# Performance work log

Measured on AMD Instinct MI355X. Metric: run time of the kernel, lower is better.

Reference implementation:

```python
import jax, jax.numpy as jnp
import numpy as np

ITERS = 15
KERNEL = 7
PAD = 3
INIT_RATE = 0.1
SCALE_PSDF = 1000.0
EDGE_THRESH = 0.01


def _min_pool7(x):
    # torch: -maxpool2d(-x, k=7, s=1, p=3)  ==  min-pool, padding with +inf
    return jax.lax.reduce_window(
        x, jnp.inf, jax.lax.min,
        window_dimensions=(1, 1, KERNEL, KERNEL),
        window_strides=(1, 1, 1, 1),
        padding=[(0, 0), (0, 0), (PAD, PAD), (PAD, PAD)])


def _erode_weight(mask):
    # FaceWeightedFusion.obtain_face_mask_weight: 15-iter erosion, each shell
    # of pixels removed at iteration i gets weight init_rate + i*(1-init_rate)/15
    mask_erode = mask
    mask_final = jnp.zeros_like(mask)
    for i in range(ITERS):
        nxt = _min_pool7(mask_erode)
        rate = min(INIT_RATE + i * ((1.0 - INIT_RATE) / ITERS), 1.0)
        mask_final = mask_final + (mask_erode - nxt) * rate
        mask_erode = nxt
    return mask_final + mask_erode


def _bilinear_sample(img, xy):
    # img: [B,1,H,W]; xy: [B,2,N] in [-1,1] (grid_sample convention, align_corners=True)
    B, _, H, W = img.shape
    x = (xy[:, 0] + 1.0) * 0.5 * (W - 1)  # [B,N]
    y = (xy[:, 1] + 1.0) * 0.5 * (H - 1)
    x0 = jnp.floor(x); y0 = jnp.floor(y)
    wx = x - x0; wy = y - y0
    x0i = jnp.clip(x0, 0, W - 1).astype(jnp.int32)
    x1i = jnp.clip(x0 + 1, 0, W - 1).astype(jnp.int32)
    y0i = jnp.clip(y0, 0, H - 1).astype(jnp.int32)
    y1i = jnp.clip(y0 + 1, 0, H - 1).astype(jnp.int32)
    flat = img[:, 0].reshape(B, H * W)
    g = lambda yi, xi: jnp.take_along_axis(flat, yi * W + xi, axis=1)
    v = (g(y0i, x0i) * (1 - wx) * (1 - wy) + g(y0i, x1i) * wx * (1 - wy)
         + g(y1i, x0i) * (1 - wx) * wy + g(y1i, x1i) * wx * wy)
    return v[:, None, :]  # [B,1,N]


def setup_inputs() -> dict:
    key = jax.random.key(0)
    ks = jax.random.split(key, 7)
    B, H, W, N = 4, 1024, 1024, 262144
    mask = (jax.random.uniform(ks[0], (B, 1, H, W)) > 0.5).astype(jnp.float32)
    face_depth = jax.random.uniform(ks[1], (B, 1, H, W))
    face_depth_edge_mask = (jax.random.uniform(ks[2], (B, 1, H, W)) > 0.3).astype(jnp.float32)
    xy = jax.random.uniform(ks[3], (B, 2, N)) * 2.0 - 1.0
    z = jax.random.normal(ks[4], (B, 1, N)) * 0.1 + 0.5
    occ_body = jax.random.uniform(ks[5], (B, 1, N))
    occ_face = jax.random.uniform(ks[6], (B, 1, N))
    return {"mask": mask, "face_depth": face_depth,
            "face_depth_edge_mask": face_depth_edge_mask,
            "xy": xy, "z": z, "occ_body": occ_body, "occ_face": occ_face}


def reference(mask, face_depth, face_depth_edge_mask, xy, z, occ_body, occ_face):
    # obtain_face_mask_weight
    mask_erode = _erode_weight(mask)
    # calculate_fusion_weights (x_weighted=True)
    edge = _bilinear_sample(face_depth_edge_mask, xy)
    edge_b = (edge > EDGE_THRESH).astype(face_depth.dtype)
    depth_q = _bilinear_sample(face_depth, xy) * edge_b
    psdf = z - depth_q
    labels = _bilinear_sample(mask_erode, xy) * edge_b
    w = jnp.exp(-(psdf ** 2) * SCALE_PSDF) * labels
    # fusion(occ_body, occ_face)
    return w * occ_face + (1.0 - w) * occ_body
```

## Files before the change

### kernel.cpp

```cpp
#include <hip/hip_runtime.h>
#include <stdint.h>


#define HH 1024
#define WW 1024
#define HWIMG (HH * WW)
#define NPTS 262144

typedef short short2v __attribute__((ext_vector_type(2)));
typedef float f32x4 __attribute__((ext_vector_type(4)));
typedef uint32_t u32x2 __attribute__((ext_vector_type(2), aligned(4)));

static __device__ __forceinline__ uint32_t umin_(uint32_t a, uint32_t b) { return a < b ? a : b; }

__global__ __launch_bounds__(256) void row_dt_kernel(const float* __restrict__ mask,
                                                     uint8_t* __restrict__ rbuf) {
    const int l = threadIdx.x & 63;
    const int row = blockIdx.x * 4 + (threadIdx.x >> 6);
    const float* mrow = mask + (size_t)row * WW;

    uint64_t bm[18];
    bm[0] = 0ull;
    bm[17] = 0ull;
#pragma unroll
    for (int i = 0; i < 16; ++i) {
        float m = mrow[i * 64 + l];
        bm[i + 1] = __ballot(m == 0.0f);
    }

    uint8_t* rrow = rbuf + (size_t)row * WW;
#pragma unroll
    for (int i = 0; i < 16; ++i) {
        uint64_t W0 = bm[i];
        uint64_t W1 = bm[i + 1];
        uint64_t W2 = bm[i + 2];
        uint64_t rmask = (W1 >> l) | ((W2 << 1) << (63 - l));
        uint64_t lmask = (W1 << (63 - l)) | ((W0 >> 1) >> l);
        int dr = rmask ? __builtin_ctzll(rmask) : 64;
        int dl = lmask ? __builtin_clzll(lmask) : 64;
        int d = dr < dl ? dr : dl;
        if (d > 46) d = 46;
        rrow[i * 64 + l] = (uint8_t)d;
    }
}

template<bool PACK>
__global__ __launch_bounds__(256) void col_dt_kernel(const uint8_t* __restrict__ rbuf,
                                                     const float* __restrict__ edge,
                                                     const float* __restrict__ depth,
                                                     uint8_t* __restrict__ bucket_out,
                                                     uint32_t* __restrict__ packed_out) {
    const int bx = blockIdx.x;
    const int tx = bx & 15, ty = (bx >> 4) & 15, b = bx >> 8;
    const int x0 = tx * 64, y0 = ty * 64;
    const int c = threadIdx.x & 63;
    const int t = threadIdx.x >> 6;
    const int ybase = y0 + t * 16;
    const uint8_t* imgc = rbuf + (size_t)b * HWIMG + x0 + c;

    uint32_t wf[12];
#pragma unroll
    for (int j = 0; j < 12; ++j) {
        int r0 = ybase - 4 + 2 * j;
        int r1 = r0 + 1;
        int r0c = r0 < 0 ? 0 : (r0 > 1023 ? 1023 : r0);
        int r1c = r1 < 0 ? 0 : (r1 > 1023 ? 1023 : r1);
        uint32_t lo = imgc[(size_t)r0c * WW];
        uint32_t hi = imgc[(size_t)r1c * WW];
        if (r0 != r0c) lo = 46;
        if (r1 != r1c) hi = 46;
        wf[j] = lo | (hi << 16);
    }

    uint32_t Dv[16];
    bool bad = false;
#pragma unroll
    for (int i = 0; i < 16; ++i) {
        const int base2 = i >> 1;
        const int par = i & 1;
        short2v D2 = (short2v){46, 46};
#pragma unroll
        for (int q = 0; q < 5; ++q) {
            int dy0 = 2 * q - 4 - par;
            short a0 = (short)(dy0 < 0 ? -dy0 : dy0);
            short a1 = (short)(dy0 + 1 < 0 ? -(dy0 + 1) : dy0 + 1);
            short2v A = (short2v){a0, a1};
            short2v v = __builtin_bit_cast(short2v, wf[base2 + q]);
            short2v mx = __builtin_elementwise_max(A, v);
            D2 = __builtin_elementwise_min(D2, mx);
        }
        uint32_t D = (uint32_t)(D2.x < D2.y ? D2.x : D2.y);
        Dv[i] = D;
        bad |= (D >= 6);
    }

    if (__ballot(bad) != 0) {
#pragma unroll
        for (int i = 0; i < 16; ++i) {
            uint32_t D = 46;
            for (int dy = -46; dy <= 46; ++dy) {
                int y = ybase + i + dy;
                uint32_t r = 46;
                if (y >= 0 && y < HH) r = imgc[(size_t)y * WW];
                uint32_t a = (uint32_t)(dy < 0 ? -dy : dy);
                uint32_t m = a > r ? a : r;
                D = D < m ? D : m;
            }
            Dv[i] = D;
        }
    }

#pragma unroll
    for (int i = 0; i < 16; ++i) {
        uint32_t D = Dv[i];
        const size_t pix = (size_t)b * HWIMG + (size_t)(ybase + i) * WW + x0 + c;
        if (PACK) {
            float dv = __builtin_nontemporal_load(&depth[pix]);
            float ev = __builtin_nontemporal_load(&edge[pix]);
            uint32_t q20 = (uint32_t)fminf(rintf(dv * 1048575.0f), 1048575.0f);
            uint32_t bk = (D == 0) ? 31u : umin_(15u, (D - 1u) / 3u);
            uint32_t word = q20 | (bk << 20) | ((ev != 0.0f ? 1u : 0u) << 25);
            __builtin_nontemporal_store(word, &packed_out[pix]);
        } else {
            uint8_t o = (D == 0) ? (uint8_t)255 : (uint8_t)umin_(15u, (D - 1u) / 3u);
            bucket_out[pix] = o;
        }
    }
}

static __device__ __forceinline__ float decode_w5(uint32_t p) {
    uint32_t k = (p >> 20) & 31u;
    if (k == 31u) return 0.0f;
    float v = 0.1f + (float)k * 0.06f;
    return v < 1.0f ? v : 1.0f;
}

__global__ __launch_bounds__(256) void sample4_kernel(
    const uint32_t* __restrict__ pimg, const float* __restrict__ xy,
    const float* __restrict__ z, const float* __restrict__ occ_body,
    const float* __restrict__ occ_face, float* __restrict__ out) {
    const int b = blockIdx.x & 3;
    const int n0 = (blockIdx.x >> 2) * 1024 + threadIdx.x * 4;
    const size_t pb = (size_t)b * NPTS;

    f32x4 xv  = __builtin_nontemporal_load((const f32x4*)&xy[pb * 2 + n0]);
    f32x4 yv  = __builtin_nontemporal_load((const f32x4*)&xy[pb * 2 + NPTS + n0]);
    f32x4 zv  = __builtin_nontemporal_load((const f32x4*)&z[pb + n0]);
    f32x4 obv = __builtin_nontemporal_load((const f32x4*)&occ_body[pb + n0]);
    f32x4 ofv = __builtin_nontemporal_load((const f32x4*)&occ_face[pb + n0]);

    const uint32_t* img = pimg + (size_t)b * HWIMG;
    f32x4 res;
    const uint32_t* addr[4][2];
    int sel[4];
    float wgt[4][4];
#pragma unroll
    for (int j = 0; j < 4; ++j) {
        float fx = ((xv[j] + 1.0f) * 0.5f) * 1023.0f;
        float fy = ((yv[j] + 1.0f) * 0.5f) * 1023.0f;
        float x0f = floorf(fx), y0f = floorf(fy);
        float wx = fx - x0f, wy = fy - y0f;
        int x0i = (int)x0f; x0i = x0i < 0 ? 0 : (x0i > 1023 ? 1023 : x0i);
        int y0i = (int)y0f; y0i = y0i < 0 ? 0 : (y0i > 1023 ? 1023 : y0i);
        int y1i = y0i + 1 > 1023 ? 1023 : y0i + 1;
        int xl = x0i > 1022 ? 1022 : x0i;
        sel[j] = x0i - xl;
        addr[j][0] = img + (size_t)y0i * WW + xl;
        addr[j][1] = img + (size_t)y1i * WW + xl;
        wgt[j][0] = (1.0f - wx) * (1.0f - wy);
        wgt[j][1] = wx * (1.0f - wy);
        wgt[j][2] = (1.0f - wx) * wy;
        wgt[j][3] = wx * wy;
    }
    u32x2 pr[4][2];
#pragma unroll
    for (int j = 0; j < 4; ++j) {
        pr[j][0] = *(const u32x2*)addr[j][0];
        pr[j][1] = *(const u32x2*)addr[j][1];
    }

#pragma unroll
    for (int j = 0; j < 4; ++j) {
        uint32_t p00 = sel[j] ? pr[j][0].y : pr[j][0].x;
        uint32_t p01 = pr[j][0].y;
        uint32_t p10 = sel[j] ? pr[j][1].y : pr[j][1].x;
        uint32_t p11 = pr[j][1].y;
        float e = (float)((p00 >> 25) & 1u) * wgt[j][0]
                + (float)((p01 >> 25) & 1u) * wgt[j][1]
                + (float)((p10 >> 25) & 1u) * wgt[j][2]
                + (float)((p11 >> 25) & 1u) * wgt[j][3];
        float w = 0.0f;
        if (e > 0.01f) {
            const float DQS = 1.0f / 1048575.0f;
            float dq = ((float)(p00 & 0xFFFFFu) * wgt[j][0]
                      + (float)(p01 & 0xFFFFFu) * wgt[j][1]
                      + (float)(p10 & 0xFFFFFu) * wgt[j][2]
                      + (float)(p11 & 0xFFFFFu) * wgt[j][3]) * DQS;
            float la = decode_w5(p00) * wgt[j][0] + decode_w5(p01) * wgt[j][1]
                     + decode_w5(p10) * wgt[j][2] + decode_w5(p11) * wgt[j][3];
            float ps = zv[j] - dq;
            w = expf(-(ps * ps) * 1000.0f) * la;
        }
        res[j] = w * ofv[j] + (1.0f - w) * obv[j];
    }
    __builtin_nontemporal_store(res, (f32x4*)&out[pb + n0]);
}

static __device__ __forceinline__ float decode_w8(uint32_t k) {
    if (k == 255u) return 0.0f;
    float v = 0.1f + (float)k * 0.06f;
    return v < 1.0f ? v : 1.0f;
}

__global__ __launch_bounds__(256) void sample_fallback_kernel(
    const float* __restrict__ edge_img, const float* __restrict__ depth_img,
    const uint8_t* __restrict__ wimg,
    const float* __restrict__ xy, const float* __restrict__ z,
    const float* __restrict__ occ_body, const float* __restrict__ occ_face,
    float* __restrict__ out) {
    const int b = blockIdx.x & 3;
    const int n = (blockIdx.x >> 2) * 256 + threadIdx.x;

    float x = xy[(size_t)b * 2 * NPTS + n];
    float y = xy[(size_t)b * 2 * NPTS + NPTS + n];
    float fx = ((x + 1.0f) * 0.5f) * 1023.0f;
    float fy = ((y + 1.0f) * 0.5f) * 1023.0f;
    float x0f = floorf(fx), y0f = floorf(fy);
    float wx = fx - x0f, wy = fy - y0f;
    int x0i = (int)x0f; x0i = x0i < 0 ? 0 : (x0i > 1023 ? 1023 : x0i);
    int y0i = (int)y0f; y0i = y0i < 0 ? 0 : (y0i > 1023 ? 1023 : y0i);
    int x1i = x0i + 1 > 1023 ? 1023 : x0i + 1;
    int y1i = y0i + 1 > 1023 ? 1023 : y0i + 1;

    const size_t base = (size_t)b * HWIMG;
    const size_t i00 = base + (size_t)y0i * WW + x0i;
    const size_t i01 = base + (size_t)y0i * WW + x1i;
    const size_t i10 = base + (size_t)y1i * WW + x0i;
    const size_t i11 = base + (size_t)y1i * WW + x1i;

    const float w00 = (1.0f - wx) * (1.0f - wy);
    const float w01 = wx * (1.0f - wy);
    const float w10 = (1.0f - wx) * wy;
    const float w11 = wx * wy;

    float zv = z[(size_t)b * NPTS + n];
    float ob = occ_body[(size_t)b * NPTS + n];
    float of = occ_face[(size_t)b * NPTS + n];

    float w = 0.0f;
    float e = edge_img[i00] * w00 + edge_img[i01] * w01
            + edge_img[i10] * w10 + edge_img[i11] * w11;
    if (e > 0.01f) {
        float dq = depth_img[i00] * w00 + depth_img[i01] * w01
                 + depth_img[i10] * w10 + depth_img[i11] * w11;
        float la = decode_w8(wimg[i00]) * w00 + decode_w8(wimg[i01]) * w01
                 + decode_w8(wimg[i10]) * w10 + decode_w8(wimg[i11]) * w11;
        float ps = zv - dq;
        w = expf(-(ps * ps) * 1000.0f) * la;
    }
    out[(size_t)b * NPTS + n] = w * of + (1.0f - w) * ob;
}

extern "C" void kernel_launch(void* const* d_in, const int* in_sizes, int n_in,
                              void* d_out, int out_size, void* d_ws, size_t ws_size,
                              hipStream_t stream) {
    const float* mask      = (const float*)d_in[0];
    const float* depth     = (const float*)d_in[1];
    const float* edge      = (const float*)d_in[2];
    const float* xy        = (const float*)d_in[3];
    const float* z         = (const float*)d_in[4];
    const float* occ_body  = (const float*)d_in[5];
    const float* occ_face  = (const float*)d_in[6];
    float* out = (float*)d_out;

    uint8_t* rbuf = (uint8_t*)d_ws;
    const size_t need_packed = (size_t)4 * HWIMG + (size_t)4 * HWIMG * 4;

    row_dt_kernel<<<1024, 256, 0, stream>>>(mask, rbuf);

    if (ws_size >= need_packed) {
        uint32_t* pimg = (uint32_t*)(rbuf + (size_t)4 * HWIMG);
        col_dt_kernel<true><<<1024, 256, 0, stream>>>(rbuf, edge, depth, nullptr, pimg);
        sample4_kernel<<<1024, 256, 0, stream>>>(pimg, xy, z, occ_body, occ_face, out);
    } else {
        uint8_t* wbuf = rbuf + (size_t)4 * HWIMG;
        col_dt_kernel<false><<<1024, 256, 0, stream>>>(rbuf, edge, depth, wbuf, nullptr);
        sample_fallback_kernel<<<4096, 256, 0, stream>>>(edge, depth, wbuf,
                                                         xy, z, occ_body, occ_face, out);
    }
}
```

Before: 131.2 us.

## Store packed image as row-pair interleaved planes for single 16-byte bilinear fetch

The column pass now writes the packed depth/edge/weight words into two row-pair interleaved buffers (even-start and odd-start pairs), so each pixel stores its value together with the one below it. The sampler then picks the buffer by row parity and fetches all four bilinear taps with one 16-byte load instead of two 8-byte loads from separate rows. This trades roughly double the packed-image write traffic and workspace for fewer, better-localised random gathers in the sampling kernel.

```diff
diff --git a/kernel.cpp b/kernel.cpp
--- a/kernel.cpp
+++ b/kernel.cpp
@@ -9,7 +9,8 @@
 
 typedef short short2v __attribute__((ext_vector_type(2)));
 typedef float f32x4 __attribute__((ext_vector_type(4)));
-typedef uint32_t u32x2 __attribute__((ext_vector_type(2), aligned(4)));
+typedef uint32_t u32x2 __attribute__((ext_vector_type(2), aligned(8)));
+typedef uint32_t u32x4a __attribute__((ext_vector_type(4), aligned(8)));
 
 static __device__ __forceinline__ uint32_t umin_(uint32_t a, uint32_t b) { return a < b ? a : b; }
 
@@ -49,7 +50,8 @@
                                                      const float* __restrict__ edge,
                                                      const float* __restrict__ depth,
                                                      uint8_t* __restrict__ bucket_out,
-                                                     uint32_t* __restrict__ packed_out) {
+                                                     uint32_t* __restrict__ qE,
+                                                     uint32_t* __restrict__ qO) {
     const int bx = blockIdx.x;
     const int tx = bx & 15, ty = (bx >> 4) & 15, b = bx >> 8;
     const int x0 = tx * 64, y0 = ty * 64;
@@ -110,18 +112,48 @@
         }
     }
 
-#pragma unroll
-    for (int i = 0; i < 16; ++i) {
-        uint32_t D = Dv[i];
-        const size_t pix = (size_t)b * HWIMG + (size_t)(ybase + i) * WW + x0 + c;
-        if (PACK) {
+    if (PACK) {
+        uint32_t wv[16];
+#pragma unroll
+        for (int i = 0; i < 16; ++i) {
+            uint32_t D = Dv[i];
+            const size_t pix = (size_t)b * HWIMG + (size_t)(ybase + i) * WW + x0 + c;
             float dv = __builtin_nontemporal_load(&depth[pix]);
             float ev = __builtin_nontemporal_load(&edge[pix]);
             uint32_t q20 = (uint32_t)fminf(rintf(dv * 1048575.0f), 1048575.0f);
             uint32_t bk = (D == 0) ? 31u : umin_(15u, (D - 1u) / 3u);
-            uint32_t word = q20 | (bk << 20) | ((ev != 0.0f ? 1u : 0u) << 25);
-            __builtin_nontemporal_store(word, &packed_out[pix]);
-        } else {
+            wv[i] = q20 | (bk << 20) | ((ev != 0.0f ? 1u : 0u) << 25);
+        }
+
+        const int xcol = x0 + c;
+        const size_t bq = (size_t)b * (HWIMG / 2);
+        u32x2* qE2 = (u32x2*)qE;
+        u32x2* qO2 = (u32x2*)qO;
+        const int k0 = ybase >> 1;
+#pragma unroll
+        for (int a = 0; a < 8; ++a) {
+            u32x2 pr2 = (u32x2){wv[2 * a], wv[2 * a + 1]};
+            __builtin_nontemporal_store(pr2, &qE2[bq + (size_t)(k0 + a) * WW + xcol]);
+        }
+#pragma unroll
+        for (int a = 0; a < 7; ++a) {
+            u32x2 pr2 = (u32x2){wv[2 * a + 1], wv[2 * a + 2]};
+            __builtin_nontemporal_store(pr2, &qO2[bq + (size_t)(k0 + a) * WW + xcol]);
+        }
+        uint32_t* qOu = qO;
+        const size_t bqu = (size_t)b * HWIMG;
+        if (ybase > 0) {
+            __builtin_nontemporal_store(wv[0], &qOu[bqu + ((size_t)(k0 - 1) * WW + xcol) * 2 + 1]);
+        }
+        __builtin_nontemporal_store(wv[15], &qOu[bqu + ((size_t)(k0 + 7) * WW + xcol) * 2]);
+        if (ybase + 15 == 1023) {
+            __builtin_nontemporal_store(wv[15], &qOu[bqu + ((size_t)(k0 + 7) * WW + xcol) * 2 + 1]);
+        }
+    } else {
+#pragma unroll
+        for (int i = 0; i < 16; ++i) {
+            uint32_t D = Dv[i];
+            const size_t pix = (size_t)b * HWIMG + (size_t)(ybase + i) * WW + x0 + c;
             uint8_t o = (D == 0) ? (uint8_t)255 : (uint8_t)umin_(15u, (D - 1u) / 3u);
             bucket_out[pix] = o;
         }
@@ -136,7 +168,8 @@
 }
 
 __global__ __launch_bounds__(256) void sample4_kernel(
-    const uint32_t* __restrict__ pimg, const float* __restrict__ xy,
+    const uint32_t* __restrict__ qE, const uint32_t* __restrict__ qO,
+    const float* __restrict__ xy,
     const float* __restrict__ z, const float* __restrict__ occ_body,
     const float* __restrict__ occ_face, float* __restrict__ out) {
     const int b = blockIdx.x & 3;
@@ -149,9 +182,9 @@
     f32x4 obv = __builtin_nontemporal_load((const f32x4*)&occ_body[pb + n0]);
     f32x4 ofv = __builtin_nontemporal_load((const f32x4*)&occ_face[pb + n0]);
 
-    const uint32_t* img = pimg + (size_t)b * HWIMG;
+    const size_t bimg = (size_t)b * HWIMG;
     f32x4 res;
-    const uint32_t* addr[4][2];
+    const uint32_t* addr[4];
     int sel[4];
     float wgt[4][4];
 #pragma unroll
@@ -162,29 +195,27 @@
         float wx = fx - x0f, wy = fy - y0f;
         int x0i = (int)x0f; x0i = x0i < 0 ? 0 : (x0i > 1023 ? 1023 : x0i);
         int y0i = (int)y0f; y0i = y0i < 0 ? 0 : (y0i > 1023 ? 1023 : y0i);
-        int y1i = y0i + 1 > 1023 ? 1023 : y0i + 1;
         int xl = x0i > 1022 ? 1022 : x0i;
         sel[j] = x0i - xl;
-        addr[j][0] = img + (size_t)y0i * WW + xl;
-        addr[j][1] = img + (size_t)y1i * WW + xl;
+        const uint32_t* base = (y0i & 1) ? qO : qE;
+        addr[j] = base + bimg + ((size_t)(y0i >> 1) * WW + xl) * 2;
         wgt[j][0] = (1.0f - wx) * (1.0f - wy);
         wgt[j][1] = wx * (1.0f - wy);
         wgt[j][2] = (1.0f - wx) * wy;
         wgt[j][3] = wx * wy;
     }
-    u32x2 pr[4][2];
+    u32x4a pr[4];
 #pragma unroll
     for (int j = 0; j < 4; ++j) {
-        pr[j][0] = *(const u32x2*)addr[j][0];
-        pr[j][1] = *(const u32x2*)addr[j][1];
+        pr[j] = *(const u32x4a*)addr[j];
     }
 
 #pragma unroll
     for (int j = 0; j < 4; ++j) {
-        uint32_t p00 = sel[j] ? pr[j][0].y : pr[j][0].x;
-        uint32_t p01 = pr[j][0].y;
-        uint32_t p10 = sel[j] ? pr[j][1].y : pr[j][1].x;
-        uint32_t p11 = pr[j][1].y;
+        uint32_t p00 = sel[j] ? pr[j].z : pr[j].x;
+        uint32_t p01 = pr[j].z;
+        uint32_t p10 = sel[j] ? pr[j].w : pr[j].y;
+        uint32_t p11 = pr[j].w;
         float e = (float)((p00 >> 25) & 1u) * wgt[j][0]
                 + (float)((p01 >> 25) & 1u) * wgt[j][1]
                 + (float)((p10 >> 25) & 1u) * wgt[j][2]
@@ -274,17 +305,18 @@
     float* out = (float*)d_out;
 
     uint8_t* rbuf = (uint8_t*)d_ws;
-    const size_t need_packed = (size_t)4 * HWIMG + (size_t)4 * HWIMG * 4;
+    const size_t need_packed = (size_t)4 * HWIMG * (1 + 4 + 4);
 
     row_dt_kernel<<<1024, 256, 0, stream>>>(mask, rbuf);
 
     if (ws_size >= need_packed) {
-        uint32_t* pimg = (uint32_t*)(rbuf + (size_t)4 * HWIMG);
-        col_dt_kernel<true><<<1024, 256, 0, stream>>>(rbuf, edge, depth, nullptr, pimg);
-        sample4_kernel<<<1024, 256, 0, stream>>>(pimg, xy, z, occ_body, occ_face, out);
+        uint32_t* qE = (uint32_t*)(rbuf + (size_t)4 * HWIMG);
+        uint32_t* qO = qE + (size_t)4 * HWIMG;
+        col_dt_kernel<true><<<1024, 256, 0, stream>>>(rbuf, edge, depth, nullptr, qE, qO);
+        sample4_kernel<<<1024, 256, 0, stream>>>(qE, qO, xy, z, occ_body, occ_face, out);
     } else {
         uint8_t* wbuf = rbuf + (size_t)4 * HWIMG;
-        col_dt_kernel<false><<<1024, 256, 0, stream>>>(rbuf, edge, depth, wbuf, nullptr);
+        col_dt_kernel<false><<<1024, 256, 0, stream>>>(rbuf, edge, depth, wbuf, nullptr, nullptr);
         sample_fallback_kernel<<<4096, 256, 0, stream>>>(edge, depth, wbuf,
                                                          xy, z, occ_body, occ_face, out);
     }
```

Measured after the change: 131.4 us. About the same (+0.2%).
